# Kernel tuning notes

Hardware: AMD Instinct MI355X
Metric: run time of the kernel (lower is better)

The kernel has to match this reference:

```python
import jax, jax.numpy as jnp
import numpy as np

WS = 7
B, Dd, Hh, Wd, C, NH = 1, 28, 28, 28, 384, 12

def _rel_index(ws):
    coords = np.stack(np.meshgrid(np.arange(ws), np.arange(ws), np.arange(ws), indexing='ij'))
    cf = coords.reshape(3, -1)
    rel = (cf[:, :, None] - cf[:, None, :]).transpose(1, 2, 0) + (ws - 1)
    rel[:, :, 0] *= (2 * ws - 1) ** 2
    rel[:, :, 1] *= (2 * ws - 1)
    return rel.sum(-1)  # (ws^3, ws^3)

REL_IDX = _rel_index(WS)

def setup_inputs():
    key = jax.random.key(0)
    ks = jax.random.split(key, 8)
    L = Dd * Hh * Wd
    s = 0.02
    return {
        'skip': jax.random.normal(ks[0], (B, L, C), jnp.float32),
        'x_up': jax.random.normal(ks[1], (B, L, C), jnp.float32),
        'D': Dd, 'H': Hh, 'W': Wd,
        'ln1_g': jnp.ones((C,), jnp.float32), 'ln1_b': jnp.zeros((C,), jnp.float32),
        'kv_w': jax.random.normal(ks[2], (C, 2 * C), jnp.float32) * s,
        'kv_b': jnp.zeros((2 * C,), jnp.float32),
        'rpb': jax.random.normal(ks[3], ((2 * WS - 1) ** 3, NH), jnp.float32) * s,
        'proj_w': jax.random.normal(ks[4], (C, C), jnp.float32) * s,
        'proj_b': jnp.zeros((C,), jnp.float32),
        'ln2_g': jnp.ones((C,), jnp.float32), 'ln2_b': jnp.zeros((C,), jnp.float32),
        'mlp_w1': jax.random.normal(ks[5], (C, 4 * C), jnp.float32) * s,
        'mlp_b1': jnp.zeros((4 * C,), jnp.float32),
        'mlp_w2': jax.random.normal(ks[6], (4 * C, C), jnp.float32) * s,
        'mlp_b2': jnp.zeros((C,), jnp.float32),
    }

def _ln(x, g, b):
    m = jnp.mean(x, -1, keepdims=True)
    v = jnp.mean(jnp.square(x - m), -1, keepdims=True)
    return (x - m) * jax.lax.rsqrt(v + 1e-5) * g + b

def _win_part(x):
    b, d, h, w, c = x.shape
    x = x.reshape(b, d // WS, WS, h // WS, WS, w // WS, WS, c)
    return x.transpose(0, 1, 3, 5, 2, 4, 6, 7).reshape(-1, WS ** 3, c)

def _win_rev(x, b, d, h, w):
    c = x.shape[-1]
    x = x.reshape(b, d // WS, h // WS, w // WS, WS, WS, WS, c)
    return x.transpose(0, 1, 4, 2, 5, 3, 6, 7).reshape(b, d, h, w, c)

def reference(skip, x_up, D, H, W, ln1_g, ln1_b, kv_w, kv_b, rpb, proj_w, proj_b, ln2_g, ln2_b, mlp_w1, mlp_b1, mlp_w2, mlp_b2):
    b, L, c = skip.shape
    x = x_up + skip  # wrapper residual; shortcut of the inner block
    # inner block was built with shift_size=0 -> no cyclic shift, attn_mask unused
    sk = _win_part(_ln(skip, ln1_g, ln1_b).reshape(b, D, H, W, c))   # (nW, N, C) -> K,V source
    qx = _win_part(_ln(x_up, ln1_g, ln1_b).reshape(b, D, H, W, c))   # (nW, N, C) -> Q source
    nW, N, _ = sk.shape
    hd = c // NH
    kv = (sk @ kv_w + kv_b).reshape(nW, N, 2, NH, hd)
    k, v = kv[:, :, 0], kv[:, :, 1]                  # (nW, N, NH, hd)
    q = qx.reshape(nW, N, NH, hd) * (hd ** -0.5)     # no q projection in WindowAttention_kv
    attn = jnp.einsum('wqhd,wkhd->whqk', q, k)
    bias = rpb[REL_IDX.reshape(-1)].reshape(N, N, NH).transpose(2, 0, 1)
    attn = jax.nn.softmax(attn + bias[None], axis=-1)
    o = jnp.einsum('whqk,wkhd->wqhd', attn, v).reshape(nW, N, c)
    o = o @ proj_w + proj_b
    o = _win_rev(o, b, D, H, W).reshape(b, L, c)
    x = x + o
    h1 = jax.nn.gelu(_ln(x, ln2_g, ln2_b) @ mlp_w1 + mlp_b1)
    x = x + h1 @ mlp_w2 + mlp_b2
    return x
```

## Files before the change

### kernel.cpp

```cpp
#include <hip/hip_runtime.h>
#include <hip/hip_bf16.h>
#include <cstdint>

typedef unsigned short u16;
typedef short s16x8 __attribute__((ext_vector_type(8)));
typedef short s16x4 __attribute__((ext_vector_type(4)));
typedef float f32x4 __attribute__((ext_vector_type(4)));

#define C_DIM 384
#define NHEAD 12
#define HD    32
#define NTOK  343
#define NWIN  64
#define LTOT  21952
#define SIDE  28

__device__ __forceinline__ float u2f(u16 u) {
    return __uint_as_float(((unsigned int)u) << 16);
}
__device__ __forceinline__ u16 f2b(float f) {
    unsigned int u = __float_as_uint(f);
    return (u16)((u + 0x7fffu + ((u >> 16) & 1u)) >> 16);
}
__device__ __forceinline__ float exp2_hw(float x) {
    float r;
    asm("v_exp_f32 %0, %1" : "=v"(r) : "v"(x));
    return r;
}
__device__ __forceinline__ unsigned int pk_bf16(float lo, float hi) {
    unsigned int r;
    asm("v_cvt_pk_bf16_f32 %0, %1, %2" : "=v"(r) : "v"(lo), "v"(hi));
    return r;
}
__device__ __forceinline__ float gelu_fast(float x) {
    float e = exp2_hw(-2.3022083f * (x + 0.044715f * x * x * x));
    return x * __builtin_amdgcn_rcpf(1.f + e);
}

__global__ __launch_bounds__(256) void k_wt(
    const float* __restrict__ W, u16* __restrict__ Wt, int K, int N)
{
    __shared__ float T[64][65];
    int k0 = blockIdx.x * 64, n0 = blockIdx.y * 64;
    int t = threadIdx.x;
    int c = t & 63, rg = t >> 6;
#pragma unroll
    for (int i = 0; i < 16; i++) {
        int r = rg * 16 + i;
        T[r][c] = W[(size_t)(k0 + r) * N + n0 + c];
    }
    __syncthreads();
    int k = t & 63, ng = t >> 6;
#pragma unroll
    for (int i = 0; i < 16; i++) {
        int n = ng * 16 + i;
        Wt[(size_t)(n0 + n) * K + k0 + k] = f2b(T[k][n]);
    }
}

__global__ __launch_bounds__(256) void k_wt_pi(
    const float* __restrict__ W, u16* __restrict__ Wt, int K, int N)
{
    __shared__ float T[64][65];
    int k0 = blockIdx.x * 64, n0 = blockIdx.y * 64;
    int t = threadIdx.x;
    int c = t & 63, rg = t >> 6;
#pragma unroll
    for (int i = 0; i < 16; i++) {
        int r = rg * 16 + i;
        T[r][c] = W[(size_t)(k0 + r) * N + n0 + c];
    }
    __syncthreads();
    int k = t & 63, ng = t >> 6;
    int kg = k0 + k;
    int j = kg & 127, ct = j >> 4, nn = j & 15;
    int kp = (kg & ~127) | ((ct >> 1) << 5) | (nn << 1) | (ct & 1);
#pragma unroll
    for (int i = 0; i < 16; i++) {
        int n = ng * 16 + i;
        Wt[(size_t)(n0 + n) * K + kp] = f2b(T[k][n]);
    }
}

__global__ __launch_bounds__(256) void k_lnprep(
    const float* __restrict__ skip, const float* __restrict__ xup,
    const float* __restrict__ g, const float* __restrict__ bta,
    u16* __restrict__ skW, u16* __restrict__ qW, u16* __restrict__ res)
{
    int t = blockIdx.x * 4 + (threadIdx.x >> 6);
    int lane = threadIdx.x & 63;
    const float* ps = skip + (size_t)t * C_DIM;
    const float* px = xup + (size_t)t * C_DIM;
    float vs[6], vx[6];
    float s1 = 0.f, s2 = 0.f, x1 = 0.f, x2 = 0.f;
#pragma unroll
    for (int j = 0; j < 6; j++) {
        float a = ps[lane + j * 64];
        float b = px[lane + j * 64];
        vs[j] = a; vx[j] = b;
        s1 += a; s2 += a * a; x1 += b; x2 += b * b;
    }
#pragma unroll
    for (int off = 32; off; off >>= 1) {
        s1 += __shfl_xor(s1, off);
        s2 += __shfl_xor(s2, off);
        x1 += __shfl_xor(x1, off);
        x2 += __shfl_xor(x2, off);
    }
    float ms = s1 * (1.f / 384.f), mx = x1 * (1.f / 384.f);
    float rs = rsqrtf(fmaxf(s2 * (1.f / 384.f) - ms * ms, 0.f) + 1e-5f);
    float rx = rsqrtf(fmaxf(x2 * (1.f / 384.f) - mx * mx, 0.f) + 1e-5f);
    int d = t / 784, rem = t % 784, hh = rem / 28, ww = rem % 28;
    int win = (d / 7) * 16 + (hh / 7) * 4 + (ww / 7);
    int n = (d % 7) * 49 + (hh % 7) * 7 + (ww % 7);
    size_t dst = ((size_t)(win * NTOK + n)) * C_DIM + lane;
    size_t td  = (size_t)t * C_DIM + lane;
#pragma unroll
    for (int j = 0; j < 6; j++) {
        int c = lane + j * 64;
        float gg = g[c], bb = bta[c];
        skW[dst + j * 64] = f2b((vs[j] - ms) * rs * gg + bb);
        qW[dst + j * 64]  = f2b((vx[j] - mx) * rx * gg + bb);
        res[td + j * 64]  = f2b(vs[j] + vx[j]);
    }
}

__global__ __launch_bounds__(256) void k_ln2(
    const u16* __restrict__ x2, const float* __restrict__ g,
    const float* __restrict__ bta, u16* __restrict__ lnx)
{
    int t = blockIdx.x * 4 + (threadIdx.x >> 6);
    int lane = threadIdx.x & 63;
    const u16* p = x2 + (size_t)t * C_DIM;
    float v[6];
    float s1 = 0.f, s2 = 0.f;
#pragma unroll
    for (int j = 0; j < 6; j++) {
        float a = u2f(p[lane + j * 64]);
        v[j] = a; s1 += a; s2 += a * a;
    }
#pragma unroll
    for (int off = 32; off; off >>= 1) {
        s1 += __shfl_xor(s1, off);
        s2 += __shfl_xor(s2, off);
    }
    float m = s1 * (1.f / 384.f);
    float r = rsqrtf(fmaxf(s2 * (1.f / 384.f) - m * m, 0.f) + 1e-5f);
    size_t dst = (size_t)t * C_DIM + lane;
#pragma unroll
    for (int j = 0; j < 6; j++) {
        int c = lane + j * 64;
        lnx[dst + j * 64] = f2b((v[j] - m) * r * g[c] + bta[c]);
    }
}

#define BPAD 40

__device__ __forceinline__ void gemm128(
    const u16* __restrict__ A, const u16* __restrict__ Bt, int K, int M,
    int rowBase, int colBase, int tid,
    u16 (*As)[BPAD], u16 (*Bs)[BPAD], f32x4 acc[4][4])
{
    const int sr  = tid >> 2;
    const int scg = (tid & 3) << 3;
    const int lane = tid & 63, wv = tid >> 6;
    const int m16 = lane & 15, quad = lane >> 4;
    const int wr = (wv >> 1) << 6, wc = (wv & 1) << 6;

    int ra0 = min(rowBase + sr, M - 1);
    int ra1 = min(rowBase + 64 + sr, M - 1);
    const u16* pa0 = A + (size_t)ra0 * K + scg;
    const u16* pa1 = A + (size_t)ra1 * K + scg;
    const u16* pb0 = Bt + (size_t)(colBase + sr) * K + scg;
    const u16* pb1 = Bt + (size_t)(colBase + 64 + sr) * K + scg;

    uint4 a0 = *(const uint4*)pa0, a1 = *(const uint4*)pa1;
    uint4 b0 = *(const uint4*)pb0, b1 = *(const uint4*)pb1;

    for (int kk = 0; kk < K; kk += 32) {
        *(uint4*)&As[sr][scg]      = a0;
        *(uint4*)&As[64 + sr][scg] = a1;
        *(uint4*)&Bs[sr][scg]      = b0;
        *(uint4*)&Bs[64 + sr][scg] = b1;
        __syncthreads();
        if (kk + 32 < K) {
            a0 = *(const uint4*)(pa0 + kk + 32);
            a1 = *(const uint4*)(pa1 + kk + 32);
            b0 = *(const uint4*)(pb0 + kk + 32);
            b1 = *(const uint4*)(pb1 + kk + 32);
        }
        s16x8 af[4], bf[4];
#pragma unroll
        for (int rt = 0; rt < 4; rt++)
            af[rt] = *(const s16x8*)&As[wr + rt * 16 + m16][quad * 8];
#pragma unroll
        for (int bt = 0; bt < 4; bt++)
            bf[bt] = *(const s16x8*)&Bs[wc + bt * 16 + m16][quad * 8];
#pragma unroll
        for (int rt = 0; rt < 4; rt++)
#pragma unroll
        for (int bt = 0; bt < 4; bt++)
            acc[rt][bt] = __builtin_amdgcn_mfma_f32_16x16x32_bf16(af[rt], bf[bt], acc[rt][bt], 0, 0, 0);
        __syncthreads();
    }
}

__device__ __forceinline__ void gemm64_db(
    const u16* __restrict__ A, const u16* __restrict__ Bt, int K, int M,
    int rowBase, int colBase, int tid,
    u16 (*As)[BPAD], u16 (*Bs)[BPAD], f32x4 acc[4][2])
{
    const int sr  = tid >> 2;
    const int scg = (tid & 3) << 3;
    const int lane = tid & 63, wv = tid >> 6;
    const int m16 = lane & 15, quad = lane >> 4;
    const int wc = wv << 5;

    int ra = min(rowBase + sr, M - 1);
    const u16* pa  = A + (size_t)ra * K + scg;
    const u16* pb0 = Bt + (size_t)(colBase + sr) * K + scg;
    const u16* pb1 = Bt + (size_t)(colBase + 64 + sr) * K + scg;

    uint4 aA = *(const uint4*)pa,        bA0 = *(const uint4*)pb0,        bA1 = *(const uint4*)pb1;
    uint4 aB = *(const uint4*)(pa + 32), bB0 = *(const uint4*)(pb0 + 32), bB1 = *(const uint4*)(pb1 + 32);

    *(uint4*)&As[sr][scg]      = aA;
    *(uint4*)&Bs[sr][scg]      = bA0;
    *(uint4*)&Bs[64 + sr][scg] = bA1;
    if (64 < K) {
        aA  = *(const uint4*)(pa + 64);
        bA0 = *(const uint4*)(pb0 + 64);
        bA1 = *(const uint4*)(pb1 + 64);
    }
    __syncthreads();

    for (int kk = 0; kk < K; kk += 64) {
        *(uint4*)&As[64 + sr][scg]  = aB;
        *(uint4*)&Bs[128 + sr][scg] = bB0;
        *(uint4*)&Bs[192 + sr][scg] = bB1;
        if (kk + 96 < K) {
            aB  = *(const uint4*)(pa  + kk + 96);
            bB0 = *(const uint4*)(pb0 + kk + 96);
            bB1 = *(const uint4*)(pb1 + kk + 96);
        }
        {
            s16x8 af[4], bf[2];
#pragma unroll
            for (int rt = 0; rt < 4; rt++)
                af[rt] = *(const s16x8*)&As[rt * 16 + m16][quad * 8];
#pragma unroll
            for (int bt = 0; bt < 2; bt++)
                bf[bt] = *(const s16x8*)&Bs[wc + bt * 16 + m16][quad * 8];
#pragma unroll
            for (int rt = 0; rt < 4; rt++)
#pragma unroll
            for (int bt = 0; bt < 2; bt++)
                acc[rt][bt] = __builtin_amdgcn_mfma_f32_16x16x32_bf16(af[rt], bf[bt], acc[rt][bt], 0, 0, 0);
        }
        __syncthreads();
        if (kk + 64 < K) {
            *(uint4*)&As[sr][scg]      = aA;
            *(uint4*)&Bs[sr][scg]      = bA0;
            *(uint4*)&Bs[64 + sr][scg] = bA1;
        }
        if (kk + 128 < K) {
            aA  = *(const uint4*)(pa  + kk + 128);
            bA0 = *(const uint4*)(pb0 + kk + 128);
            bA1 = *(const uint4*)(pb1 + kk + 128);
        }
        {
            s16x8 af[4], bf[2];
#pragma unroll
            for (int rt = 0; rt < 4; rt++)
                af[rt] = *(const s16x8*)&As[64 + rt * 16 + m16][quad * 8];
#pragma unroll
            for (int bt = 0; bt < 2; bt++)
                bf[bt] = *(const s16x8*)&Bs[128 + wc + bt * 16 + m16][quad * 8];
#pragma unroll
            for (int rt = 0; rt < 4; rt++)
#pragma unroll
            for (int bt = 0; bt < 2; bt++)
                acc[rt][bt] = __builtin_amdgcn_mfma_f32_16x16x32_bf16(af[rt], bf[bt], acc[rt][bt], 0, 0, 0);
        }
        __syncthreads();
    }
}

#define EPI_SETUP \
    int lane = tid & 63, wv = tid >> 6, quad = lane >> 4, n16 = lane & 15;

__global__ __launch_bounds__(256) void k_gemm_kv(
    const u16* __restrict__ A, const u16* __restrict__ Wt, const float* __restrict__ bias,
    u16* __restrict__ Kb, u16* __restrict__ Vb)
{
    __shared__ __align__(16) u16 As[128][BPAD];
    __shared__ __align__(16) u16 Bs[128][BPAD];
    f32x4 acc[4][4] = {};
    int tid = threadIdx.x;
    int rowBase = blockIdx.x * 128, colBase = blockIdx.y * 128;
    gemm128(A, Wt, 384, LTOT, rowBase, colBase, tid, As, Bs, acc);
    EPI_SETUP
    int wr = (wv >> 1) << 6, wc = (wv & 1) << 6;
#pragma unroll
    for (int bt = 0; bt < 4; bt++) {
        int col = colBase + wc + bt * 16 + n16;
        float bcol = bias[col];
        int isv = col >= 384;
        int remc = col - (isv ? 384 : 0);
        int hh = remc >> 5, dd = remc & 31;
#pragma unroll
        for (int rt = 0; rt < 4; rt++)
#pragma unroll
        for (int reg = 0; reg < 4; reg++) {
            int r = rowBase + wr + rt * 16 + quad * 4 + reg;
            if (r < LTOT) {
                int w = r / NTOK, nn = r % NTOK;
                size_t dst = ((size_t)((w * NHEAD + hh) * NTOK + nn)) * HD + dd;
                (isv ? Vb : Kb)[dst] = f2b(acc[rt][bt][reg] + bcol);
            }
        }
    }
}

__global__ __launch_bounds__(256) void k_gemm_proj(
    const u16* __restrict__ A, const u16* __restrict__ Wt, const float* __restrict__ bias,
    const u16* __restrict__ res, u16* __restrict__ x2)
{
    __shared__ __align__(16) u16 As[128][BPAD];
    __shared__ __align__(16) u16 Bs[256][BPAD];
    f32x4 acc[4][2] = {};
    int tid = threadIdx.x;
    int rowBase = blockIdx.x * 64, colBase = blockIdx.y * 128;
    gemm64_db(A, Wt, 384, LTOT, rowBase, colBase, tid, As, Bs, acc);
    EPI_SETUP
    int wc = wv << 5;
#pragma unroll
    for (int bt = 0; bt < 2; bt++) {
        int col = colBase + wc + bt * 16 + n16;
        float bcol = bias[col];
#pragma unroll
        for (int rt = 0; rt < 4; rt++)
#pragma unroll
        for (int reg = 0; reg < 4; reg++) {
            int r = rowBase + rt * 16 + quad * 4 + reg;
            if (r < LTOT) {
                size_t idx = (size_t)r * C_DIM + col;
                x2[idx] = f2b(acc[rt][bt][reg] + bcol + u2f(res[idx]));
            }
        }
    }
}

__global__ __launch_bounds__(256) void k_gemm_mlp1(
    const u16* __restrict__ A, const u16* __restrict__ Wt, const float* __restrict__ bias,
    u16* __restrict__ h1c, int rowOfs)
{
    __shared__ __align__(16) u16 As[128][BPAD];
    __shared__ __align__(16) u16 Bs[128][BPAD];
    f32x4 acc[4][4] = {};
    int tid = threadIdx.x;
    int rowBase = rowOfs + blockIdx.x * 128, colBase = blockIdx.y * 128;
    gemm128(A, Wt, 384, LTOT, rowBase, colBase, tid, As, Bs, acc);
    EPI_SETUP
    int wr = (wv >> 1) << 6;
#pragma unroll
    for (int p2 = 0; p2 < 2; p2++) {
        int p = (wv & 1) * 2 + p2;
        int col0 = colBase + p * 32 + n16;
        int col1 = col0 + 16;
        float bc0 = bias[col0], bc1 = bias[col1];
        int dcol = colBase + p * 32 + 2 * n16;
#pragma unroll
        for (int rt = 0; rt < 4; rt++)
#pragma unroll
        for (int reg = 0; reg < 4; reg++) {
            int r = rowBase + wr + rt * 16 + quad * 4 + reg;
            if (r < LTOT) {
                size_t rl = (size_t)(r - rowOfs);
                float v0 = gelu_fast(acc[rt][2 * p2][reg] + bc0);
                float v1 = gelu_fast(acc[rt][2 * p2 + 1][reg] + bc1);
                *(unsigned int*)&h1c[rl * 1536 + dcol] = pk_bf16(v0, v1);
            }
        }
    }
}

__global__ __launch_bounds__(256) void k_gemm_mlp2(
    const u16* __restrict__ A, const u16* __restrict__ Wt, const float* __restrict__ bias,
    const u16* __restrict__ x2, float* __restrict__ out, int rowOfs, int chunkRows)
{
    __shared__ __align__(16) u16 As[128][BPAD];
    __shared__ __align__(16) u16 Bs[256][BPAD];
    f32x4 acc[4][2] = {};
    int tid = threadIdx.x;
    int rowBase = blockIdx.x * 64, colBase = blockIdx.y * 128;
    gemm64_db(A, Wt, 1536, chunkRows, rowBase, colBase, tid, As, Bs, acc);
    EPI_SETUP
    int wc = wv << 5;
#pragma unroll
    for (int bt = 0; bt < 2; bt++) {
        int col = colBase + wc + bt * 16 + n16;
        float bcol = bias[col];
#pragma unroll
        for (int rt = 0; rt < 4; rt++)
#pragma unroll
        for (int reg = 0; reg < 4; reg++) {
            int rl = rowBase + rt * 16 + quad * 4 + reg;
            int rg = rowOfs + rl;
            if (rl < chunkRows && rg < LTOT) {
                size_t idx = (size_t)rg * C_DIM + col;
                out[idx] = acc[rt][bt][reg] + bcol + u2f(x2[idx]);
            }
        }
    }
}

#define VP  360
#define PBS 36

__global__ __launch_bounds__(256, 2) void k_attn(
    const u16* __restrict__ qW, const u16* __restrict__ Kb, const u16* __restrict__ Vb,
    const float* __restrict__ rpb, u16* __restrict__ oT)
{
    __shared__ __align__(16) u16 Vt[32 * VP];
    __shared__ __align__(16) u16 rp16[2200];
    __shared__ __align__(16) u16 code[352];
    __shared__ __align__(16) u16 Pb[4 * 16 * PBS];

    const int h = blockIdx.x, w = blockIdx.y;
    const int tid = threadIdx.x;
    const int lane = tid & 63, wv = tid >> 6;
    const int m16 = lane & 15, quad = lane >> 4;
    const size_t base = ((size_t)(w * NHEAD + h)) * NTOK * HD;
    const u16* Kg = Kb + base;

    for (int t = tid; t < 704; t += 256) {
        int dg = t / 176, rem = t - dg * 176;
        int kb = rem >> 4, j = rem & 15;
        int n0 = kb * 32 + j, n1 = n0 + 16;
        uint4 uA = make_uint4(0, 0, 0, 0), uB = make_uint4(0, 0, 0, 0);
        if (n0 < NTOK) uA = *(const uint4*)(Vb + base + n0 * HD + dg * 8);
        if (n1 < NTOK) uB = *(const uint4*)(Vb + base + n1 * HD + dg * 8);
        int d0 = dg * 8, colu = kb * 32 + 2 * j;
        unsigned int pk0 = (uA.x & 0xffffu) | (uB.x << 16);
        unsigned int pk1 = (uA.x >> 16)     | (uB.x & 0xffff0000u);
        unsigned int pk2 = (uA.y & 0xffffu) | (uB.y << 16);
        unsigned int pk3 = (uA.y >> 16)     | (uB.y & 0xffff0000u);
        unsigned int pk4 = (uA.z & 0xffffu) | (uB.z << 16);
        unsigned int pk5 = (uA.z >> 16)     | (uB.z & 0xffff0000u);
        unsigned int pk6 = (uA.w & 0xffffu) | (uB.w << 16);
        unsigned int pk7 = (uA.w >> 16)     | (uB.w & 0xffff0000u);
        *(unsigned int*)&Vt[(d0 + 0) * VP + colu] = pk0;
        *(unsigned int*)&Vt[(d0 + 1) * VP + colu] = pk1;
        *(unsigned int*)&Vt[(d0 + 2) * VP + colu] = pk2;
        *(unsigned int*)&Vt[(d0 + 3) * VP + colu] = pk3;
        *(unsigned int*)&Vt[(d0 + 4) * VP + colu] = pk4;
        *(unsigned int*)&Vt[(d0 + 5) * VP + colu] = pk5;
        *(unsigned int*)&Vt[(d0 + 6) * VP + colu] = pk6;
        *(unsigned int*)&Vt[(d0 + 7) * VP + colu] = pk7;
    }
    for (int t = tid; t < 2200; t += 256)
        rp16[t] = (t < 2197) ? f2b(rpb[t * NHEAD + h] * 1.4426950408889634f) : (u16)0;
    for (int t = tid; t < 352; t += 256) {
        int z = t / 49, rem = t % 49, y = rem / 7, x = rem % 7;
        code[t] = (t < NTOK) ? (u16)(z * 169 + y * 13 + x) : (u16)1098;
    }
    __syncthreads();

    const float scale = 0.2550348772f;
    u16* myP = Pb + wv * 16 * PBS;

    for (int qt = wv; qt < 22; qt += 4) {
        int qbase = qt * 16;
        int qrow = min(qbase + m16, NTOK - 1);
        s16x8 qf = *(const s16x8*)(qW + ((size_t)(w * NTOK + qrow)) * C_DIM
                                       + h * HD + quad * 8);
        int qcv[4];
#pragma unroll
        for (int i = 0; i < 4; i++) qcv[i] = code[qbase + quad * 4 + i];

        f32x4 S0[11], S1[11];
        float mx[4] = {-1e30f, -1e30f, -1e30f, -1e30f};

#pragma unroll
        for (int ks = 0; ks < 11; ks++) {
            int kbase = ks * 32;
            int kt0 = kbase + m16, kt1 = kt0 + 16;
            s16x8 kf0 = *(const s16x8*)(Kg + (size_t)kt0 * HD + quad * 8);
            s16x8 kf1 = *(const s16x8*)(Kg + (size_t)kt1 * HD + quad * 8);
            f32x4 z = {0.f, 0.f, 0.f, 0.f};
            f32x4 sA = __builtin_amdgcn_mfma_f32_16x16x32_bf16(qf, kf0, z, 0, 0, 0);
            f32x4 sB = __builtin_amdgcn_mfma_f32_16x16x32_bf16(qf, kf1, z, 0, 0, 0);
            int kc0 = code[kt0], kc1 = code[kt1];
            bool k1ok = (ks < 10) || (kt1 < NTOK);
#pragma unroll
            for (int i = 0; i < 4; i++) {
                float b0 = u2f(rp16[qcv[i] - kc0 + 1098]);
                float b1 = u2f(rp16[qcv[i] - kc1 + 1098]);
                float sa = fmaf(sA[i], scale, b0);
                float sb = k1ok ? fmaf(sB[i], scale, b1) : -1e30f;
                S0[ks][i] = sa;
                S1[ks][i] = sb;
                mx[i] = fmaxf(mx[i], fmaxf(sa, sb));
            }
        }
#pragma unroll
        for (int i = 0; i < 4; i++) {
            float v = mx[i];
            v = fmaxf(v, __shfl_xor(v, 1));
            v = fmaxf(v, __shfl_xor(v, 2));
            v = fmaxf(v, __shfl_xor(v, 4));
            v = fmaxf(v, __shfl_xor(v, 8));
            mx[i] = v;
        }

        f32x4 O0 = {}, O1 = {};
        float l[4] = {};
#pragma unroll
        for (int ks = 0; ks < 11; ks++) {
            int kbase = ks * 32;
#pragma unroll
            for (int i = 0; i < 4; i++) {
                float pa = exp2_hw(S0[ks][i] - mx[i]);
                float pb = exp2_hw(S1[ks][i] - mx[i]);
                l[i] += pa + pb;
                *(unsigned int*)&myP[(quad * 4 + i) * PBS + 2 * m16] = pk_bf16(pa, pb);
            }
            s16x4 plo = *(const s16x4*)&myP[m16 * PBS + quad * 8];
            s16x4 phi = *(const s16x4*)&myP[m16 * PBS + quad * 8 + 4];
            s16x8 pf  = __builtin_shufflevector(plo, phi, 0, 1, 2, 3, 4, 5, 6, 7);
            s16x8 vf0 = *(const s16x8*)&Vt[m16 * VP + kbase + quad * 8];
            s16x8 vf1 = *(const s16x8*)&Vt[(16 + m16) * VP + kbase + quad * 8];
            O0 = __builtin_amdgcn_mfma_f32_16x16x32_bf16(pf, vf0, O0, 0, 0, 0);
            O1 = __builtin_amdgcn_mfma_f32_16x16x32_bf16(pf, vf1, O1, 0, 0, 0);
        }
#pragma unroll
        for (int i = 0; i < 4; i++) {
            float v = l[i];
            v += __shfl_xor(v, 1);
            v += __shfl_xor(v, 2);
            v += __shfl_xor(v, 4);
            v += __shfl_xor(v, 8);
            l[i] = v;
        }

        int wd = w >> 4, wh = (w >> 2) & 3, wwi = w & 3;
#pragma unroll
        for (int i = 0; i < 4; i++) {
            int q = qbase + quad * 4 + i;
            if (q < NTOK) {
                float rl = __builtin_amdgcn_rcpf(l[i]);
                int qz = q / 49, qrem = q % 49, qy = qrem / 7, qx = qrem % 7;
                size_t tok = ((size_t)(wd * 7 + qz) * SIDE + (wh * 7 + qy)) * SIDE
                             + (wwi * 7 + qx);
                u16* op = oT + tok * C_DIM + h * HD;
                op[m16]      = f2b(O0[i] * rl);
                op[16 + m16] = f2b(O1[i] * rl);
            }
        }
    }
}

extern "C" void kernel_launch(void* const* d_in, const int* in_sizes, int n_in,
                              void* d_out, int out_size, void* d_ws, size_t ws_size,
                              hipStream_t stream)
{
    const float* skip = (const float*)d_in[0];
    const float* xup  = (const float*)d_in[1];
    const float* ln1g = (const float*)d_in[5];
    const float* ln1b = (const float*)d_in[6];
    const float* kvw  = (const float*)d_in[7];
    const float* kvb  = (const float*)d_in[8];
    const float* rpb  = (const float*)d_in[9];
    const float* pw   = (const float*)d_in[10];
    const float* pb   = (const float*)d_in[11];
    const float* ln2g = (const float*)d_in[12];
    const float* ln2b = (const float*)d_in[13];
    const float* w1   = (const float*)d_in[14];
    const float* b1   = (const float*)d_in[15];
    const float* w2   = (const float*)d_in[16];
    const float* b2   = (const float*)d_in[17];
    float* out = (float*)d_out;

    char* ws = (char*)d_ws;
    const size_t BUFB = (size_t)LTOT * C_DIM * 2;
    const size_t WTB  = 589824 + 294912 + 1179648 + 1179648;
    u16* skW = (u16*)(ws);
    u16* qW  = (u16*)(ws + BUFB);
    u16* Kb  = (u16*)(ws + 2 * BUFB);
    u16* Vb  = (u16*)(ws + 3 * BUFB);
    u16* oT  = (u16*)(ws);
    u16* x2  = (u16*)(ws + BUFB);
    u16* lnx = (u16*)(ws + 2 * BUFB);
    char* wt = ws + 4 * BUFB;
    u16* kvWt = (u16*)(wt);
    u16* pWt  = (u16*)(wt + 589824);
    u16* w1t  = (u16*)(wt + 589824 + 294912);
    u16* w2t  = (u16*)(wt + 589824 + 294912 + 1179648);
    u16* res  = (u16*)d_out;

    const size_t used = 4 * BUFB + WTB;
    const size_t blkBytes = 128 * 1536 * 2;
    size_t tailCap = (ws_size > used) ? (ws_size - used) / blkBytes : 0;
    int chunkBlocks;
    u16* h1c;
    if (tailCap >= 43) {
        chunkBlocks = tailCap < 172 ? (int)tailCap : 172;
        h1c = (u16*)(ws + used);
    } else {
        chunkBlocks = 42;
        h1c = (u16*)(ws + 3 * BUFB);
    }

    k_wt<<<dim3(6, 12), 256, 0, stream>>>(kvw, kvWt, 384, 768);
    k_wt<<<dim3(6, 6),  256, 0, stream>>>(pw,  pWt,  384, 384);
    k_wt<<<dim3(6, 24), 256, 0, stream>>>(w1,  w1t,  384, 1536);
    k_wt_pi<<<dim3(24, 6), 256, 0, stream>>>(w2, w2t, 1536, 384);

    k_lnprep<<<LTOT / 4, 256, 0, stream>>>(skip, xup, ln1g, ln1b, skW, qW, res);
    k_gemm_kv<<<dim3(172, 6), 256, 0, stream>>>(skW, kvWt, kvb, Kb, Vb);
    k_attn<<<dim3(NHEAD, NWIN), 256, 0, stream>>>(qW, Kb, Vb, rpb, oT);
    k_gemm_proj<<<dim3(343, 3), 256, 0, stream>>>(oT, pWt, pb, res, x2);
    k_ln2<<<LTOT / 4, 256, 0, stream>>>(x2, ln2g, ln2b, lnx);
    for (int b0 = 0; b0 < 172; b0 += chunkBlocks) {
        int nb = (172 - b0) < chunkBlocks ? (172 - b0) : chunkBlocks;
        int rowOfs = b0 * 128;
        int chunkRows = nb * 128;
        if (rowOfs + chunkRows > LTOT) chunkRows = LTOT - rowOfs;
        int nb64 = (chunkRows + 63) / 64;
        k_gemm_mlp1<<<dim3(nb, 12), 256, 0, stream>>>(lnx, w1t, b1, h1c, rowOfs);
        k_gemm_mlp2<<<dim3(nb64, 3), 256, 0, stream>>>(h1c, w2t, b2, x2, out, rowOfs, chunkRows);
    }
}
```

Before: 436.9 us.

## Precompute dense bias plane and fold q scale into LN output

Adds a kernel that builds a per-head 352x352 bf16 relative-position bias table (pre-multiplied by log2e) in workspace. The attention kernel feeds this bias as the MFMA accumulator initial value instead of doing gathered LDS lookups plus an FMA per score. The query scaling is moved into the LN1 prep kernel so the scores need no multiply. This drops the shared-memory rp16/code tables and their setup, at the cost of an extra 3MB bias read from global/L2 per block and an extra launch.

New measurement: 423.1 us. -3.2%, faster.

```diff
diff --git a/kernel.cpp b/kernel.cpp
--- a/kernel.cpp
+++ b/kernel.cpp
@@ -81,6 +81,24 @@
         Wt[(size_t)(n0 + n) * K + kp] = f2b(T[k][n]);
     }
 }
+
+__global__ __launch_bounds__(256) void k_bias(
+    const float* __restrict__ rpb, u16* __restrict__ biasPl)
+{
+    int h = blockIdx.x, q = blockIdx.y;
+    int qc = min(q, NTOK - 1);
+    int qz = qc / 49, qrem = qc % 49, qy = qrem / 7, qx = qrem % 7;
+    int cq = qz * 169 + qy * 13 + qx;
+    u16* dst = biasPl + ((size_t)h * 352 + q) * 352;
+    for (int k = threadIdx.x; k < 352; k += 256) {
+        int kc = min(k, NTOK - 1);
+        int kz = kc / 49, krem = kc % 49, ky = krem / 7, kx = krem % 7;
+        int ck = kz * 169 + ky * 13 + kx;
+        dst[k] = f2b(rpb[(size_t)(cq - ck + 1098) * NHEAD + h] * 1.4426950408889634f);
+    }
+}
+
+#define QSCALE 0.2550348772f
 
 __global__ __launch_bounds__(256) void k_lnprep(
     const float* __restrict__ skip, const float* __restrict__ xup,
@@ -120,7 +138,7 @@
         int c = lane + j * 64;
         float gg = g[c], bb = bta[c];
         skW[dst + j * 64] = f2b((vs[j] - ms) * rs * gg + bb);
-        qW[dst + j * 64]  = f2b((vx[j] - mx) * rx * gg + bb);
+        qW[dst + j * 64]  = f2b(((vx[j] - mx) * rx * gg + bb) * QSCALE);
         res[td + j * 64]  = f2b(vs[j] + vx[j]);
     }
 }
@@ -420,11 +438,9 @@
 
 __global__ __launch_bounds__(256, 2) void k_attn(
     const u16* __restrict__ qW, const u16* __restrict__ Kb, const u16* __restrict__ Vb,
-    const float* __restrict__ rpb, u16* __restrict__ oT)
+    const u16* __restrict__ biasPl, u16* __restrict__ oT)
 {
     __shared__ __align__(16) u16 Vt[32 * VP];
-    __shared__ __align__(16) u16 rp16[2200];
-    __shared__ __align__(16) u16 code[352];
     __shared__ __align__(16) u16 Pb[4 * 16 * PBS];
 
     const int h = blockIdx.x, w = blockIdx.y;
@@ -459,15 +475,8 @@
         *(unsigned int*)&Vt[(d0 + 6) * VP + colu] = pk6;
         *(unsigned int*)&Vt[(d0 + 7) * VP + colu] = pk7;
     }
-    for (int t = tid; t < 2200; t += 256)
-        rp16[t] = (t < 2197) ? f2b(rpb[t * NHEAD + h] * 1.4426950408889634f) : (u16)0;
-    for (int t = tid; t < 352; t += 256) {
-        int z = t / 49, rem = t % 49, y = rem / 7, x = rem % 7;
-        code[t] = (t < NTOK) ? (u16)(z * 169 + y * 13 + x) : (u16)1098;
-    }
     __syncthreads();
 
-    const float scale = 0.2550348772f;
     u16* myP = Pb + wv * 16 * PBS;
 
     for (int qt = wv; qt < 22; qt += 4) {
@@ -475,9 +484,7 @@
         int qrow = min(qbase + m16, NTOK - 1);
         s16x8 qf = *(const s16x8*)(qW + ((size_t)(w * NTOK + qrow)) * C_DIM
                                        + h * HD + quad * 8);
-        int qcv[4];
-#pragma unroll
-        for (int i = 0; i < 4; i++) qcv[i] = code[qbase + quad * 4 + i];
+        const u16* bp = biasPl + ((size_t)h * 352 + qbase + quad * 4) * 352;
 
         f32x4 S0[11], S1[11];
         float mx[4] = {-1e30f, -1e30f, -1e30f, -1e30f};
@@ -488,17 +495,19 @@
             int kt0 = kbase + m16, kt1 = kt0 + 16;
             s16x8 kf0 = *(const s16x8*)(Kg + (size_t)kt0 * HD + quad * 8);
             s16x8 kf1 = *(const s16x8*)(Kg + (size_t)kt1 * HD + quad * 8);
-            f32x4 z = {0.f, 0.f, 0.f, 0.f};
-            f32x4 sA = __builtin_amdgcn_mfma_f32_16x16x32_bf16(qf, kf0, z, 0, 0, 0);
-            f32x4 sB = __builtin_amdgcn_mfma_f32_16x16x32_bf16(qf, kf1, z, 0, 0, 0);
-            int kc0 = code[kt0], kc1 = code[kt1];
+            f32x4 c0, c1;
+#pragma unroll
+            for (int i = 0; i < 4; i++) {
+                c0[i] = u2f(bp[i * 352 + kt0]);
+                c1[i] = u2f(bp[i * 352 + kt1]);
+            }
+            f32x4 sA = __builtin_amdgcn_mfma_f32_16x16x32_bf16(qf, kf0, c0, 0, 0, 0);
+            f32x4 sB = __builtin_amdgcn_mfma_f32_16x16x32_bf16(qf, kf1, c1, 0, 0, 0);
             bool k1ok = (ks < 10) || (kt1 < NTOK);
 #pragma unroll
             for (int i = 0; i < 4; i++) {
-                float b0 = u2f(rp16[qcv[i] - kc0 + 1098]);
-                float b1 = u2f(rp16[qcv[i] - kc1 + 1098]);
-                float sa = fmaf(sA[i], scale, b0);
-                float sb = k1ok ? fmaf(sB[i], scale, b1) : -1e30f;
+                float sa = sA[i];
+                float sb = k1ok ? sB[i] : -1e30f;
                 S0[ks][i] = sa;
                 S1[ks][i] = sb;
                 mx[i] = fmaxf(mx[i], fmaxf(sa, sb));
@@ -585,6 +594,7 @@
     char* ws = (char*)d_ws;
     const size_t BUFB = (size_t)LTOT * C_DIM * 2;
     const size_t WTB  = 589824 + 294912 + 1179648 + 1179648;
+    const size_t BIASB = (size_t)NHEAD * 352 * 352 * 2;
     u16* skW = (u16*)(ws);
     u16* qW  = (u16*)(ws + BUFB);
     u16* Kb  = (u16*)(ws + 2 * BUFB);
@@ -597,9 +607,10 @@
     u16* pWt  = (u16*)(wt + 589824);
     u16* w1t  = (u16*)(wt + 589824 + 294912);
     u16* w2t  = (u16*)(wt + 589824 + 294912 + 1179648);
+    u16* biasPl = (u16*)(wt + WTB);
     u16* res  = (u16*)d_out;
 
-    const size_t used = 4 * BUFB + WTB;
+    const size_t used = 4 * BUFB + WTB + BIASB;
     const size_t blkBytes = 128 * 1536 * 2;
     size_t tailCap = (ws_size > used) ? (ws_size - used) / blkBytes : 0;
     int chunkBlocks;
@@ -616,10 +627,11 @@
     k_wt<<<dim3(6, 6),  256, 0, stream>>>(pw,  pWt,  384, 384);
     k_wt<<<dim3(6, 24), 256, 0, stream>>>(w1,  w1t,  384, 1536);
     k_wt_pi<<<dim3(24, 6), 256, 0, stream>>>(w2, w2t, 1536, 384);
+    k_bias<<<dim3(NHEAD, 352), 256, 0, stream>>>(rpb, biasPl);
 
     k_lnprep<<<LTOT / 4, 256, 0, stream>>>(skip, xup, ln1g, ln1b, skW, qW, res);
     k_gemm_kv<<<dim3(172, 6), 256, 0, stream>>>(skW, kvWt, kvb, Kb, Vb);
-    k_attn<<<dim3(NHEAD, NWIN), 256, 0, stream>>>(qW, Kb, Vb, rpb, oT);
+    k_attn<<<dim3(NHEAD, NWIN), 256, 0, stream>>>(qW, Kb, Vb, biasPl, oT);
     k_gemm_proj<<<dim3(343, 3), 256, 0, stream>>>(oT, pWt, pb, res, x2);
     k_ln2<<<LTOT / 4, 256, 0, stream>>>(x2, ln2g, ln2b, lnx);
     for (int b0 = 0; b0 < 172; b0 += chunkBlocks) {
```
